# Kernel tuning notes

Measured on AMD Instinct MI355X. Metric: run time of the kernel, lower is better.

## Reference

```python
import jax, jax.numpy as jnp
import numpy as np

B, T, Fd, C, D = 16, 256, 128, 32, 32
K_RATIO = 0.5
EPS = 1e-5


def setup_inputs() -> dict:
    key = jax.random.key(0)
    ks = jax.random.split(key, 40)
    n = lambda i, shape, s=0.05: jax.random.normal(ks[i], shape, jnp.float32) * s
    inp = {"x": jax.random.normal(ks[0], (B, T, Fd, C), jnp.float32)}
    inp.update(c1w=n(1, (C, C)), c1b=n(2, (C,)), bng=1.0 + n(3, (C,)), bnb=n(4, (C,)),
               bnm=n(5, (C,)), bnv=jax.random.uniform(ks[6], (C,)) + 0.5,
               c2w=n(7, (1, C)), c2b=n(8, (1,)))
    def gat_params(i0, pre):
        return {pre + "apw": n(i0, (D, C)), pre + "apb": n(i0 + 1, (D,)),
                pre + "aw": n(i0 + 2, (D,)), pre + "pww": n(i0 + 3, (D, C)),
                pre + "pwb": n(i0 + 4, (D,)), pre + "pow": n(i0 + 5, (D, C)),
                pre + "pob": n(i0 + 6, (D,)), pre + "g": 1.0 + n(i0 + 7, (D,)),
                pre + "be": n(i0 + 8, (D,)), pre + "m": n(i0 + 9, (D,)),
                pre + "v": jax.random.uniform(ks[i0 + 10], (D,)) + 0.5}
    inp.update(gat_params(9, "fc_"))
    inp.update(gat_params(20, "tc_"))
    inp.update(pfw=n(31, (1, D)), pfb=n(32, (1,)), ptw=n(33, (1, D)), ptb=n(34, (1,)),
               w1=n(35, (D, D)), w2=n(36, (D, D)), fcw=n(37, (2, 2 * D)), fcb=n(38, (2,)))
    return inp


def _gat(h, apw, apb, aw, pww, pwb, poww, pob, g, be, mu, var):
    # h: (B, N, C). Dense pairwise multiplication -> (B, N, N, C)
    p = h[:, :, None, :] * h[:, None, :, :]
    e = jnp.tanh(jnp.einsum('bijc,dc->bijd', p, apw) + apb)      # (B,N,N,D)
    att = jax.nn.softmax(jnp.einsum('bijd,d->bij', e, aw), axis=2)  # softmax over dim=-2 (temp=1)
    out = jnp.einsum('bij,bjc->bic', att, h) @ pww.T + pwb + h @ poww.T + pob
    out = (out - mu) / jnp.sqrt(var + EPS) * g + be               # BatchNorm1d (eval)
    return jax.nn.selu(out)


def _pool(h, pw, pb, ratio):
    s = jax.nn.sigmoid(h @ pw.T + pb)                # (B,N,1)
    kn = max(int(h.shape[1] * ratio), 1)
    _, idx = jax.lax.top_k(s[..., 0], kn)            # (B,kn), descending scores
    return jnp.take_along_axis(h * s, idx[..., None], axis=1)


def reference(x, c1w, c1b, bng, bnb, bnm, bnv, c2w, c2b,
              fc_apw, fc_apb, fc_aw, fc_pww, fc_pwb, fc_pow, fc_pob, fc_g, fc_be, fc_m, fc_v,
              tc_apw, tc_apb, tc_aw, tc_pww, tc_pwb, tc_pow, tc_pob, tc_g, tc_be, tc_m, tc_v,
              pfw, pfb, ptw, ptb, w1, w2, fcw, fcb):
    # conv1 (1x1), SELU, BatchNorm2d (eval), conv2 (1x1 -> 1 channel)
    xp = jnp.einsum('oc,btfc->botf', c1w, x) + c1b[None, :, None, None]
    xp = jax.nn.selu(xp)
    xp = (xp - bnm[None, :, None, None]) / jnp.sqrt(bnv + EPS)[None, :, None, None] \
         * bng[None, :, None, None] + bnb[None, :, None, None]
    m = jnp.einsum('c,bctf->btf', c2w[0], xp) + c2b[0]           # (B,T,F)
    M0 = jax.nn.softmax(m, axis=1)
    FCatt = jnp.einsum('btf,btfc->bfc', M0, x)                   # sum over T
    TCatt = jnp.einsum('btf,btfc->btc', M0, x)                   # sum over F
    FC_gat = _gat(FCatt, fc_apw, fc_apb, fc_aw, fc_pww, fc_pwb, fc_pow, fc_pob, fc_g, fc_be, fc_m, fc_v)
    TC_gat = _gat(TCatt, tc_apw, tc_apb, tc_aw, tc_pww, tc_pwb, tc_pow, tc_pob, tc_g, tc_be, tc_m, tc_v)
    xF = _pool(FC_gat, pfw, pfb, K_RATIO)                        # (B, F/2, D)
    xT = _pool(TC_gat, ptw, ptb, K_RATIO)                        # (B, T/2, D)
    M1 = jax.nn.softmax((xF @ w1.T) @ xT.transpose(0, 2, 1), axis=-1)
    M2 = jax.nn.softmax((xT @ w2.T) @ xF.transpose(0, 2, 1), axis=-1)
    xF_fused = xF + M1 @ xT
    xT_fused = xT + M2 @ xF
    node = jnp.concatenate([xF_fused.max(axis=1), xT_fused.max(axis=1)], axis=-1)
    return node @ fcw.T + fcb
```

## Files before the change

kernel.cpp:

```cpp
#include <hip/hip_runtime.h>
#include <hip/hip_bf16.h>

#define Bn 16
#define Tn 256
#define Fn 128
#define Cn 32
#define Dn 32
#define EPSf 1e-5f
#define SELU_L 1.0507009873554805f
#define SELU_A 1.6732632423543772f

typedef unsigned short u16;
typedef unsigned int u32;
typedef __attribute__((ext_vector_type(8))) short bf16x8;
typedef __attribute__((ext_vector_type(4))) float f32x4;

struct Ptrs { const void* p[39]; };

#define P_C1W 0
#define P_C1B 1024
#define P_MW  1056
#define P_MK  1088
#define P_FC  1089
#define P_TCG (1089+3264)
#define G_APW 0
#define G_APB 1024
#define G_AW  1056
#define G_PWW 1088
#define G_PWB 2112
#define G_POW 2144
#define G_POB 3168
#define G_GS  3200
#define G_GB  3232
#define GAT_SZ 3264
#define P_PFW (P_TCG+GAT_SZ)
#define P_PFB (P_PFW+32)
#define P_PTW (P_PFB+1)
#define P_PTB (P_PTW+32)
#define P_W1  (P_PTB+1)
#define P_W2  (P_W1+1024)
#define P_FCW (P_W2+1024)
#define P_FCB (P_FCW+128)
#define P_FLAG 10000

#define WS_M     10240
#define WS_FCATT (WS_M+524288)
#define WS_TCATT (WS_FCATT+65536)
#define WS_FCGAT (WS_TCATT+131072)
#define WS_TCGAT (WS_FCGAT+65536)
#define WS_XF    (WS_TCGAT+131072)
#define WS_XT    (WS_XF+32768)
#define WS_XFF   (WS_XT+65536)
#define WS_XTF   (WS_XFF+32768)

__device__ __forceinline__ float bf2f(u16 u) {
    union { u32 i; float f; } v; v.i = ((u32)u) << 16; return v.f;
}
__device__ __forceinline__ u16 f2bf(float f) {
    union { float f; u32 u; } v; v.f = f;
    u32 r = (v.u + 0x7fffu + ((v.u >> 16) & 1u)) >> 16;
    return (u16)r;
}
__device__ __forceinline__ u32 cvt_pk_bf16(float lo, float hi) {
    u32 r;
    asm("v_cvt_pk_bf16_f32 %0, %1, %2" : "=v"(r) : "v"(lo), "v"(hi));
    return r;
}
__device__ __forceinline__ void up2(u32 u, float* o) {
    union { u32 i; float f; } a, b;
    a.i = u << 16; b.i = u & 0xffff0000u;
    o[0] = a.f; o[1] = b.f;
}
__device__ __forceinline__ float tanh_fast(float x) {
    float e = __expf(2.f * x);
    return 1.f - 2.f / (e + 1.f);
}
__device__ __forceinline__ float ldp(const void* p, int i, int isb) {
    return isb ? bf2f(((const u16*)p)[i]) : ((const float*)p)[i];
}

__global__ __launch_bounds__(256) void k0_setup(Ptrs in, float* __restrict__ P) {
    __shared__ int sflag;
    int tid = threadIdx.x;
    int blk = blockIdx.x;
    if (tid < 64) {
        const u16* xu = (const u16*)in.p[0];
        int bad = 0;
        #pragma unroll
        for (int q = 0; q < 4; q++) {
            float f = bf2f(xu[tid * 4 + q]);
            float a = fabsf(f);
            if (!(a < 64.f) && !(a == 0.f)) bad++;
        }
        #pragma unroll
        for (int off = 32; off >= 1; off >>= 1) bad += __shfl_xor(bad, off, 64);
        if (tid == 0) sflag = (bad <= 8) ? 1 : 0;
    }
    __syncthreads();
    const int isb = sflag;

    if (blk == 0) {
        if (tid == 0) P[P_FLAG] = (float)isb;
        for (int i = tid; i < 1024; i += 256) P[P_C1W + i] = ldp(in.p[1], i, isb);
        if (tid < 32) {
            float A = ldp(in.p[3], tid, isb) * rsqrtf(ldp(in.p[6], tid, isb) + EPSf);
            float w = ldp(in.p[7], tid, isb);
            P[P_C1B + tid] = ldp(in.p[2], tid, isb);
            P[P_MW + tid] = w * A * SELU_L;
            float Bc = ldp(in.p[4], tid, isb) - ldp(in.p[5], tid, isb) * A;
            float term = w * Bc;
            #pragma unroll
            for (int off = 16; off >= 1; off >>= 1) term += __shfl_xor(term, off, 64);
            if (tid == 0) P[P_MK] = term + ldp(in.p[8], 0, isb);
        }
        if (tid >= 64 && tid < 96) {
            int t = tid - 64;
            P[P_PFW + t] = ldp(in.p[31], t, isb);
            P[P_PTW + t] = ldp(in.p[33], t, isb);
        }
        if (tid == 96) { P[P_PFB] = ldp(in.p[32], 0, isb); P[P_PTB] = ldp(in.p[34], 0, isb); }
        if (tid == 97) P[P_FCB]     = ldp(in.p[38], 0, isb);
        if (tid == 98) P[P_FCB + 1] = ldp(in.p[38], 1, isb);
        if (tid >= 128) P[P_FCW + (tid - 128)] = ldp(in.p[37], tid - 128, isb);
    } else if (blk <= 2) {
        int g = blk - 1;
        int ib = g ? 20 : 9;
        float* G = P + (g ? P_TCG : P_FC);
        for (int i = tid; i < 1024; i += 256) {
            G[G_APW + i] = ldp(in.p[ib + 0], i, isb);
            G[G_PWW + i] = ldp(in.p[ib + 3], i, isb);
            G[G_POW + i] = ldp(in.p[ib + 5], i, isb);
        }
        if (tid < 32) {
            G[G_APB + tid] = ldp(in.p[ib + 1], tid, isb);
            G[G_AW  + tid] = ldp(in.p[ib + 2], tid, isb);
            G[G_PWB + tid] = ldp(in.p[ib + 4], tid, isb);
            G[G_POB + tid] = ldp(in.p[ib + 6], tid, isb);
            float gs = ldp(in.p[ib + 7], tid, isb) * rsqrtf(ldp(in.p[ib + 10], tid, isb) + EPSf);
            G[G_GS + tid] = gs;
            G[G_GB + tid] = ldp(in.p[ib + 8], tid, isb) - ldp(in.p[ib + 9], tid, isb) * gs;
        }
    } else {
        for (int i = tid; i < 1024; i += 256) {
            P[P_W1 + i] = ldp(in.p[35], i, isb);
            P[P_W2 + i] = ldp(in.p[36], i, isb);
        }
    }
}

__global__ __launch_bounds__(256) void k1_conv_m(const void* __restrict__ xin,
                                                 const float* __restrict__ P,
                                                 float* __restrict__ M) {
    const int isb = __builtin_amdgcn_readfirstlane((int)P[P_FLAG]);
    int tid = threadIdx.x;
    if (isb) {
        int w = tid >> 6, lane = tid & 63;
        int n = lane & 15, g = lane >> 4, kc = g * 8;
        union { u32 u[4]; bf16x8 v; } B0, B1;
        #pragma unroll
        for (int e = 0; e < 4; e++) {
            B0.u[e] = cvt_pk_bf16(P[P_C1W + n * 32 + kc + 2 * e],
                                  P[P_C1W + n * 32 + kc + 2 * e + 1]);
            B1.u[e] = cvt_pk_bf16(P[P_C1W + (n + 16) * 32 + kc + 2 * e],
                                  P[P_C1W + (n + 16) * 32 + kc + 2 * e + 1]);
        }
        float cb0v[4], cb1v[4], mw0v[4], mw1v[4];
        #pragma unroll
        for (int r = 0; r < 4; r++) {
            cb0v[r] = P[P_C1B + g * 4 + r];
            cb1v[r] = P[P_C1B + 16 + g * 4 + r];
            mw0v[r] = P[P_MW + g * 4 + r];
            mw1v[r] = P[P_MW + 16 + g * 4 + r];
        }
        float mk = P[P_MK];
        int rowblk = blockIdx.x * 256 + w * 64;
        const u16* xp = (const u16*)xin + (size_t)rowblk * 32;
        bf16x8 a[4];
        #pragma unroll
        for (int s = 0; s < 4; s++)
            a[s] = *(const bf16x8*)(xp + ((size_t)s * 16 + n) * 32 + kc);
        #pragma unroll
        for (int s = 0; s < 4; s++) {
            f32x4 c0 = {0.f, 0.f, 0.f, 0.f}, c1 = {0.f, 0.f, 0.f, 0.f};
            c0 = __builtin_amdgcn_mfma_f32_16x16x32_bf16(B0.v, a[s], c0, 0, 0, 0);
            c1 = __builtin_amdgcn_mfma_f32_16x16x32_bf16(B1.v, a[s], c1, 0, 0, 0);
            float part = 0.f;
            #pragma unroll
            for (int r = 0; r < 4; r++) {
                float z0 = c0[r] + cb0v[r], z1 = c1[r] + cb1v[r];
                float s0 = (z0 > 0.f) ? z0 : SELU_A * (__expf(z0) - 1.f);
                float s1 = (z1 > 0.f) ? z1 : SELU_A * (__expf(z1) - 1.f);
                part = fmaf(mw0v[r], s0, part);
                part = fmaf(mw1v[r], s1, part);
            }
            part += __shfl_xor(part, 16, 64);
            part += __shfl_xor(part, 32, 64);
            if (lane < 16) M[(size_t)rowblk + s * 16 + n] = part + mk;
        }
    } else {
        int idx = blockIdx.x * 256 + tid;
        float xv[32];
        const float4* xf4 = reinterpret_cast<const float4*>((const float*)xin + (size_t)idx * 32);
        #pragma unroll
        for (int q = 0; q < 8; q++) {
            float4 v = xf4[q];
            xv[q * 4 + 0] = v.x; xv[q * 4 + 1] = v.y;
            xv[q * 4 + 2] = v.z; xv[q * 4 + 3] = v.w;
        }
        float acc = P[P_MK];
        #pragma unroll
        for (int o = 0; o < 32; o++) {
            float z = P[P_C1B + o];
            #pragma unroll
            for (int c = 0; c < 32; c++) z = fmaf(P[P_C1W + o * 32 + c], xv[c], z);
            float br = (z > 0.f) ? z : SELU_A * (__expf(z) - 1.f);
            acc = fmaf(P[P_MW + o], br, acc);
        }
        M[idx] = acc;
    }
}

__global__ __launch_bounds__(256) void k2_softmax(float* __restrict__ M,
                                                  float* __restrict__ FCzero) {
    __shared__ float wred[4][16];
    int b = blockIdx.x >> 3, fg = blockIdx.x & 7;
    int tid = threadIdx.x;
    int w = tid >> 6, lane = tid & 63;
    int fq = tid & 3, tt = tid >> 2;
    float* colb = M + (size_t)b * (Tn * Fn) + fg * 16 + fq * 4;
    float4 v[4];
    float mx[4] = {-1e30f, -1e30f, -1e30f, -1e30f};
    #pragma unroll
    for (int p = 0; p < 4; p++) {
        v[p] = *(float4*)(colb + (size_t)(tt + p * 64) * Fn);
        mx[0] = fmaxf(mx[0], v[p].x); mx[1] = fmaxf(mx[1], v[p].y);
        mx[2] = fmaxf(mx[2], v[p].z); mx[3] = fmaxf(mx[3], v[p].w);
    }
    #pragma unroll
    for (int off = 4; off <= 32; off <<= 1) {
        #pragma unroll
        for (int c = 0; c < 4; c++) mx[c] = fmaxf(mx[c], __shfl_xor(mx[c], off, 64));
    }
    if (lane < 4) {
        #pragma unroll
        for (int c = 0; c < 4; c++) wred[w][lane * 4 + c] = mx[c];
    }
    __syncthreads();
    #pragma unroll
    for (int c = 0; c < 4; c++)
        mx[c] = fmaxf(fmaxf(wred[0][fq * 4 + c], wred[1][fq * 4 + c]),
                      fmaxf(wred[2][fq * 4 + c], wred[3][fq * 4 + c]));
    float4 e[4];
    float sm[4] = {0.f, 0.f, 0.f, 0.f};
    #pragma unroll
    for (int p = 0; p < 4; p++) {
        e[p].x = __expf(v[p].x - mx[0]); sm[0] += e[p].x;
        e[p].y = __expf(v[p].y - mx[1]); sm[1] += e[p].y;
        e[p].z = __expf(v[p].z - mx[2]); sm[2] += e[p].z;
        e[p].w = __expf(v[p].w - mx[3]); sm[3] += e[p].w;
    }
    #pragma unroll
    for (int off = 4; off <= 32; off <<= 1) {
        #pragma unroll
        for (int c = 0; c < 4; c++) sm[c] += __shfl_xor(sm[c], off, 64);
    }
    __syncthreads();
    if (lane < 4) {
        #pragma unroll
        for (int c = 0; c < 4; c++) wred[w][lane * 4 + c] = sm[c];
    }
    __syncthreads();
    float inv[4];
    #pragma unroll
    for (int c = 0; c < 4; c++)
        inv[c] = 1.f / (wred[0][fq * 4 + c] + wred[1][fq * 4 + c] +
                        wred[2][fq * 4 + c] + wred[3][fq * 4 + c]);
    #pragma unroll
    for (int p = 0; p < 4; p++) {
        float4 o4 = make_float4(e[p].x * inv[0], e[p].y * inv[1],
                                e[p].z * inv[2], e[p].w * inv[3]);
        *(float4*)(colb + (size_t)(tt + p * 64) * Fn) = o4;
    }
    int gid = blockIdx.x * 256 + tid;
    for (int i = gid; i < Bn * Fn * Cn; i += 128 * 256) FCzero[i] = 0.f;
}

__global__ __launch_bounds__(256) void k3n(const void* __restrict__ xin,
                                           const float* __restrict__ M,
                                           const float* __restrict__ Pflag,
                                           float* __restrict__ FCatt,
                                           float* __restrict__ TCatt) {
    __shared__ float part[4][8][32];
    int bi = blockIdx.x;
    int b = bi >> 5, tg = bi & 31;
    int tid = threadIdx.x;
    int w = tid >> 6, lane = tid & 63;
    int cc = (tid & 3) * 8, f0 = tid >> 2;
    const int isb = __builtin_amdgcn_readfirstlane((int)Pflag[P_FLAG]);
    float fa0[8], fa1[8];
    #pragma unroll
    for (int e = 0; e < 8; e++) { fa0[e] = 0.f; fa1[e] = 0.f; }
    for (int tt = 0; tt < 8; tt++) {
        int t = tg * 8 + tt;
        const float* Mrow = M + (size_t)b * (Tn * Fn) + (size_t)t * Fn;
        float m0 = Mrow[f0], m1 = Mrow[f0 + 64];
        size_t rowoff = ((size_t)b * Tn + t) * (Fn * Cn);
        float xv0[8], xv1[8];
        if (isb) {
            const u16* xr = (const u16*)xin + rowoff + f0 * 32 + cc;
            union { u32 u[4]; bf16x8 v; } q0, q1;
            q0.v = *(const bf16x8*)xr;
            q1.v = *(const bf16x8*)(xr + 64 * 32);
            up2(q0.u[0], xv0 + 0); up2(q0.u[1], xv0 + 2);
            up2(q0.u[2], xv0 + 4); up2(q0.u[3], xv0 + 6);
            up2(q1.u[0], xv1 + 0); up2(q1.u[1], xv1 + 2);
            up2(q1.u[2], xv1 + 4); up2(q1.u[3], xv1 + 6);
        } else {
            const float* xr = (const float*)xin + rowoff + f0 * 32 + cc;
            float4 a0 = *(const float4*)xr, a1 = *(const float4*)(xr + 4);
            float4 b0 = *(const float4*)(xr + 64 * 32), b1 = *(const float4*)(xr + 64 * 32 + 4);
            xv0[0] = a0.x; xv0[1] = a0.y; xv0[2] = a0.z; xv0[3] = a0.w;
            xv0[4] = a1.x; xv0[5] = a1.y; xv0[6] = a1.z; xv0[7] = a1.w;
            xv1[0] = b0.x; xv1[1] = b0.y; xv1[2] = b0.z; xv1[3] = b0.w;
            xv1[4] = b1.x; xv1[5] = b1.y; xv1[6] = b1.z; xv1[7] = b1.w;
        }
        float tp[8];
        #pragma unroll
        for (int e = 0; e < 8; e++) {
            float p0 = xv0[e] * m0, p1 = xv1[e] * m1;
            fa0[e] += p0; fa1[e] += p1;
            tp[e] = p0 + p1;
        }
        #pragma unroll
        for (int off = 4; off <= 32; off <<= 1) {
            #pragma unroll
            for (int e = 0; e < 8; e++) tp[e] += __shfl_xor(tp[e], off, 64);
        }
        if (lane < 4) {
            #pragma unroll
            for (int e = 0; e < 8; e++) part[w][tt][lane * 8 + e] = tp[e];
        }
    }
    __syncthreads();
    {
        int tt = tid >> 5, c = tid & 31;
        float s = part[0][tt][c] + part[1][tt][c] + part[2][tt][c] + part[3][tt][c];
        TCatt[((size_t)b * Tn + tg * 8 + tt) * Cn + c] = s;
    }
    #pragma unroll
    for (int e = 0; e < 8; e++) {
        atomicAdd(&FCatt[(size_t)b * 4096 + f0 * 32 + cc + e],        fa0[e]);
        atomicAdd(&FCatt[(size_t)b * 4096 + (f0 + 64) * 32 + cc + e], fa1[e]);
    }
}

template<int NT>
__device__ __forceinline__ void gat_row(const float* __restrict__ h,
                                        const float* __restrict__ G,
                                        float* __restrict__ out,
                                        int i, int lane) {
    int n = lane & 15, g = lane >> 4, kc = g * 8;
    union { u32 u[4]; bf16x8 v; } B0, B1;
    #pragma unroll
    for (int e = 0; e < 4; e++) {
        B0.u[e] = cvt_pk_bf16(G[G_APW + n * 32 + kc + 2 * e],
                              G[G_APW + n * 32 + kc + 2 * e + 1]);
        B1.u[e] = cvt_pk_bf16(G[G_APW + (n + 16) * 32 + kc + 2 * e],
                              G[G_APW + (n + 16) * 32 + kc + 2 * e + 1]);
    }
    float awv0[4], awv1[4], abv0[4], abv1[4];
    #pragma unroll
    for (int r = 0; r < 4; r++) {
        awv0[r] = G[G_AW + g * 4 + r];
        awv1[r] = G[G_AW + 16 + g * 4 + r];
        abv0[r] = G[G_APB + g * 4 + r];
        abv1[r] = G[G_APB + 16 + g * 4 + r];
    }
    float hi[8];
    {
        const float4* hip = (const float4*)(h + (size_t)i * 32 + kc);
        float4 v0 = hip[0], v1 = hip[1];
        hi[0] = v0.x; hi[1] = v0.y; hi[2] = v0.z; hi[3] = v0.w;
        hi[4] = v1.x; hi[5] = v1.y; hi[6] = v1.z; hi[7] = v1.w;
    }
    float sc[NT];
    #pragma unroll
    for (int jt = 0; jt < NT; jt++) {
        const float4* hjp = (const float4*)(h + ((size_t)jt * 16 + n) * 32 + kc);
        float4 v0 = hjp[0], v1 = hjp[1];
        union { u32 u[4]; bf16x8 v; } A;
        A.u[0] = cvt_pk_bf16(hi[0] * v0.x, hi[1] * v0.y);
        A.u[1] = cvt_pk_bf16(hi[2] * v0.z, hi[3] * v0.w);
        A.u[2] = cvt_pk_bf16(hi[4] * v1.x, hi[5] * v1.y);
        A.u[3] = cvt_pk_bf16(hi[6] * v1.z, hi[7] * v1.w);
        f32x4 c0 = {0.f, 0.f, 0.f, 0.f}, c1 = {0.f, 0.f, 0.f, 0.f};
        c0 = __builtin_amdgcn_mfma_f32_16x16x32_bf16(B0.v, A.v, c0, 0, 0, 0);
        c1 = __builtin_amdgcn_mfma_f32_16x16x32_bf16(B1.v, A.v, c1, 0, 0, 0);
        float part = 0.f;
        #pragma unroll
        for (int r = 0; r < 4; r++) {
            part = fmaf(awv0[r], tanh_fast(c0[r] + abv0[r]), part);
            part = fmaf(awv1[r], tanh_fast(c1[r] + abv1[r]), part);
        }
        part += __shfl_xor(part, 16, 64);
        part += __shfl_xor(part, 32, 64);
        sc[jt] = part;
    }
    float mx = -1e30f;
    #pragma unroll
    for (int jt = 0; jt < NT; jt++) mx = fmaxf(mx, sc[jt]);
    #pragma unroll
    for (int off = 1; off < 16; off <<= 1) mx = fmaxf(mx, __shfl_xor(mx, off, 64));
    float sum = 0.f;
    #pragma unroll
    for (int jt = 0; jt < NT; jt++) { sc[jt] = __expf(sc[jt] - mx); sum += sc[jt]; }
    #pragma unroll
    for (int off = 1; off < 16; off <<= 1) sum += __shfl_xor(sum, off, 64);
    float inv = 1.f / sum;
    float attp[8] = {0.f, 0.f, 0.f, 0.f, 0.f, 0.f, 0.f, 0.f};
    #pragma unroll
    for (int jt = 0; jt < NT; jt++) {
        const float4* hjp = (const float4*)(h + ((size_t)jt * 16 + n) * 32 + kc);
        float4 v0 = hjp[0], v1 = hjp[1];
        float p = sc[jt];
        attp[0] = fmaf(p, v0.x, attp[0]); attp[1] = fmaf(p, v0.y, attp[1]);
        attp[2] = fmaf(p, v0.z, attp[2]); attp[3] = fmaf(p, v0.w, attp[3]);
        attp[4] = fmaf(p, v1.x, attp[4]); attp[5] = fmaf(p, v1.y, attp[5]);
        attp[6] = fmaf(p, v1.z, attp[6]); attp[7] = fmaf(p, v1.w, attp[7]);
    }
    #pragma unroll
    for (int off = 1; off < 16; off <<= 1) {
        #pragma unroll
        for (int e = 0; e < 8; e++) attp[e] += __shfl_xor(attp[e], off, 64);
    }
    #pragma unroll
    for (int e = 0; e < 8; e++) attp[e] *= inv;
    float att[32], hif[32];
    #pragma unroll
    for (int gg = 0; gg < 4; gg++) {
        #pragma unroll
        for (int e = 0; e < 8; e++) {
            att[gg * 8 + e] = __shfl(attp[e], gg << 4, 64);
            hif[gg * 8 + e] = __shfl(hi[e],  gg << 4, 64);
        }
    }
    int d = lane & 31;
    float z = G[G_PWB + d] + G[G_POB + d];
    #pragma unroll
    for (int c = 0; c < 32; c++)
        z = fmaf(G[G_PWW + d * 32 + c], att[c], fmaf(G[G_POW + d * 32 + c], hif[c], z));
    z = z * G[G_GS + d] + G[G_GB + d];
    z = SELU_L * ((z > 0.f) ? z : SELU_A * (__expf(z) - 1.f));
    if (lane < 32) out[(size_t)i * 32 + d] = z;
}

__global__ __launch_bounds__(256) void k4ab(const float* __restrict__ P,
                                            const float* __restrict__ FCatt,
                                            const float* __restrict__ TCatt,
                                            float* __restrict__ FCgat,
                                            float* __restrict__ TCgat) {
    int bi = blockIdx.x, tid = threadIdx.x;
    int w = tid >> 6, lane = tid & 63;
    if (bi < 512) {
        int b = bi >> 5, i = (bi & 31) * 4 + w;
        gat_row<8>(FCatt + (size_t)b * 4096, P + P_FC, FCgat + (size_t)b * 4096, i, lane);
    } else {
        int u = bi - 512;
        int b = u >> 6, i = (u & 63) * 4 + w;
        gat_row<16>(TCatt + (size_t)b * 8192, P + P_TCG, TCgat + (size_t)b * 8192, i, lane);
    }
}

__global__ __launch_bounds__(256) void k5_pool(const float* __restrict__ P,
                                               const float* __restrict__ FCgat,
                                               const float* __restrict__ TCgat,
                                               float* __restrict__ XF,
                                               float* __restrict__ XT) {
    __shared__ float s[256];
    int bi = blockIdx.x;
    int N, kn, b, pboff; const float* g; float* xp; const float* pw;
    if (bi < 16) { b = bi; N = 128; kn = 64;
        g = FCgat + (size_t)b * 4096; xp = XF + (size_t)b * 2048; pw = P + P_PFW; pboff = P_PFB; }
    else { b = bi - 16; N = 256; kn = 128;
        g = TCgat + (size_t)b * 8192; xp = XT + (size_t)b * 4096; pw = P + P_PTW; pboff = P_PTB; }
    int tid = threadIdx.x;
    float sv = 0.f;
    if (tid < N) {
        float z = P[pboff];
        #pragma unroll
        for (int d = 0; d < 32; d++) z = fmaf(pw[d], g[(size_t)tid * 32 + d], z);
        sv = 1.f / (1.f + __expf(-z));
        s[tid] = sv;
    }
    __syncthreads();
    if (tid < N) {
        int rank = 0;
        for (int l = 0; l < N; l++) {
            float sl = s[l];
            rank += (sl > sv) || (sl == sv && l < tid);
        }
        if (rank < kn) {
            #pragma unroll
            for (int d = 0; d < 32; d++) xp[(size_t)rank * 32 + d] = g[(size_t)tid * 32 + d] * sv;
        }
    }
}

__global__ __launch_bounds__(256) void k6_fuse(const float* __restrict__ P,
                                               const float* __restrict__ XF,
                                               const float* __restrict__ XT,
                                               float* __restrict__ XFF,
                                               float* __restrict__ XTF) {
    int wid = blockIdx.x * 4 + (threadIdx.x >> 6);
    int lane = threadIdx.x & 63;
    if (wid < 1024) {
        int b = wid >> 6, i = wid & 63;
        const float* xf  = XF + ((size_t)b * 64 + i) * 32;
        const float* xtb = XT + (size_t)b * 4096;
        const float* w1 = P + P_W1;
        int d = lane & 31;
        float y = 0.f;
        #pragma unroll
        for (int c = 0; c < 32; c++) y = fmaf(w1[d * 32 + c], xf[c], y);
        float xtr0[32], xtr1[32];
        #pragma unroll
        for (int c = 0; c < 32; c++) {
            xtr0[c] = xtb[(size_t)lane * 32 + c];
            xtr1[c] = xtb[(size_t)(lane + 64) * 32 + c];
        }
        float s0 = 0.f, s1 = 0.f;
        #pragma unroll
        for (int c = 0; c < 32; c++) {
            float yc = __shfl(y, c, 64);
            s0 = fmaf(yc, xtr0[c], s0);
            s1 = fmaf(yc, xtr1[c], s1);
        }
        float mx = fmaxf(s0, s1);
        #pragma unroll
        for (int off = 1; off < 64; off <<= 1) mx = fmaxf(mx, __shfl_xor(mx, off, 64));
        float e0 = __expf(s0 - mx), e1 = __expf(s1 - mx);
        float sm = e0 + e1;
        #pragma unroll
        for (int off = 1; off < 64; off <<= 1) sm += __shfl_xor(sm, off, 64);
        float inv = 1.f / sm;
        float a0 = e0 * inv, a1 = e1 * inv;
        float v[32];
        #pragma unroll
        for (int c = 0; c < 32; c++) v[c] = a0 * xtr0[c] + a1 * xtr1[c];
        #pragma unroll
        for (int off = 1; off < 64; off <<= 1) {
            #pragma unroll
            for (int c = 0; c < 32; c++) v[c] += __shfl_xor(v[c], off, 64);
        }
        if (lane == 0) {
            float* o = XFF + ((size_t)b * 64 + i) * 32;
            #pragma unroll
            for (int c = 0; c < 32; c++) o[c] = xf[c] + v[c];
        }
    } else {
        int r = wid - 1024;
        int b = r >> 7, i = r & 127;
        const float* xt  = XT + ((size_t)b * 128 + i) * 32;
        const float* xfb = XF + (size_t)b * 2048;
        const float* w2 = P + P_W2;
        int d = lane & 31;
        float y = 0.f;
        #pragma unroll
        for (int c = 0; c < 32; c++) y = fmaf(w2[d * 32 + c], xt[c], y);
        float xfr[32];
        #pragma unroll
        for (int c = 0; c < 32; c++) xfr[c] = xfb[(size_t)lane * 32 + c];
        float sc0 = 0.f;
        #pragma unroll
        for (int c = 0; c < 32; c++) sc0 = fmaf(__shfl(y, c, 64), xfr[c], sc0);
        float mx = sc0;
        #pragma unroll
        for (int off = 1; off < 64; off <<= 1) mx = fmaxf(mx, __shfl_xor(mx, off, 64));
        float e = __expf(sc0 - mx);
        float sm = e;
        #pragma unroll
        for (int off = 1; off < 64; off <<= 1) sm += __shfl_xor(sm, off, 64);
        float a = e / sm;
        float v[32];
        #pragma unroll
        for (int c = 0; c < 32; c++) v[c] = a * xfr[c];
        #pragma unroll
        for (int off = 1; off < 64; off <<= 1) {
            #pragma unroll
            for (int c = 0; c < 32; c++) v[c] += __shfl_xor(v[c], off, 64);
        }
        if (lane == 0) {
            float* o = XTF + ((size_t)b * 128 + i) * 32;
            #pragma unroll
            for (int c = 0; c < 32; c++) o[c] = xt[c] + v[c];
        }
    }
}

__global__ __launch_bounds__(64) void k7_out(const float* __restrict__ P,
                                             const float* __restrict__ XFF,
                                             const float* __restrict__ XTF,
                                             void* __restrict__ outp) {
    __shared__ float node[64];
    int b = blockIdx.x, tid = threadIdx.x;
    if (tid < 32) {
        float m = -1e30f;
        for (int r = 0; r < 64; r++) m = fmaxf(m, XFF[((size_t)b * 64 + r) * 32 + tid]);
        node[tid] = m;
    } else {
        int c = tid - 32;
        float m = -1e30f;
        for (int r = 0; r < 128; r++) m = fmaxf(m, XTF[((size_t)b * 128 + r) * 32 + c]);
        node[tid] = m;
    }
    __syncthreads();
    if (tid < 2) {
        float z = P[P_FCB + tid];
        #pragma unroll
        for (int k = 0; k < 64; k++) z = fmaf(P[P_FCW + tid * 64 + k], node[k], z);
        int isb = (int)P[P_FLAG];
        if (isb) ((u16*)outp)[b * 2 + tid] = f2bf(z);
        else     ((float*)outp)[b * 2 + tid] = z;
    }
}

extern "C" void kernel_launch(void* const* d_in, const int* in_sizes, int n_in,
                              void* d_out, int out_size, void* d_ws, size_t ws_size,
                              hipStream_t stream) {
    (void)in_sizes; (void)n_in; (void)out_size; (void)ws_size;
    float* W = (float*)d_ws;
    Ptrs ptrs;
    for (int i = 0; i < 39; i++) ptrs.p[i] = d_in[i];
    const void* x = d_in[0];
    float* P = W;

    k0_setup<<<4, 256, 0, stream>>>(ptrs, P);
    k1_conv_m<<<2048, 256, 0, stream>>>(x, P, W + WS_M);
    k2_softmax<<<128, 256, 0, stream>>>(W + WS_M, W + WS_FCATT);
    k3n<<<512, 256, 0, stream>>>(x, W + WS_M, P, W + WS_FCATT, W + WS_TCATT);
    k4ab<<<1536, 256, 0, stream>>>(P, W + WS_FCATT, W + WS_TCATT,
                                   W + WS_FCGAT, W + WS_TCGAT);
    k5_pool<<<32, 256, 0, stream>>>(P, W + WS_FCGAT, W + WS_TCGAT, W + WS_XF, W + WS_XT);
    k6_fuse<<<768, 256, 0, stream>>>(P, W + WS_XF, W + WS_XT, W + WS_XFF, W + WS_XTF);
    k7_out<<<16, 64, 0, stream>>>(P, W + WS_XFF, W + WS_XTF, d_out);
}
```

Measured before the change: 344.6 us.

## Split GAT attention rows across waves and coalesce FCatt atomics via LDS

The GAT kernel now splits each attention row's neighbour columns across 2 or 4 waves. Each wave computes a partial softmax (max, sum, weighted h) and one wave merges the partials through LDS in a flash-style rescale. The grid grows from 1536 to 5120 blocks to raise parallelism and shorten per-wave serial chains. In k3n, the per-thread FCatt partials are staged in LDS and written back with contiguous atomics, to improve atomic coalescing. This costs an extra 16KB of LDS in k3n and a block barrier, with idle waves during the merge step in k4ab.

Result: faster. 314.2 us (-8.8%).

```diff
diff --git a/kernel.cpp b/kernel.cpp
--- a/kernel.cpp
+++ b/kernel.cpp
@@ -291,6 +291,7 @@
                                            float* __restrict__ FCatt,
                                            float* __restrict__ TCatt) {
     __shared__ float part[4][8][32];
+    __shared__ __align__(16) float sh[4096];
     int bi = blockIdx.x;
     int b = bi >> 5, tg = bi & 31;
     int tid = threadIdx.x;
@@ -341,6 +342,11 @@
             for (int e = 0; e < 8; e++) part[w][tt][lane * 8 + e] = tp[e];
         }
     }
+    float4* sh4 = (float4*)sh;
+    sh4[tid * 2]       = make_float4(fa0[0], fa0[1], fa0[2], fa0[3]);
+    sh4[tid * 2 + 1]   = make_float4(fa0[4], fa0[5], fa0[6], fa0[7]);
+    sh4[512 + tid * 2]     = make_float4(fa1[0], fa1[1], fa1[2], fa1[3]);
+    sh4[512 + tid * 2 + 1] = make_float4(fa1[4], fa1[5], fa1[6], fa1[7]);
     __syncthreads();
     {
         int tt = tid >> 5, c = tid & 31;
@@ -348,25 +354,41 @@
         TCatt[((size_t)b * Tn + tg * 8 + tt) * Cn + c] = s;
     }
     #pragma unroll
-    for (int e = 0; e < 8; e++) {
-        atomicAdd(&FCatt[(size_t)b * 4096 + f0 * 32 + cc + e],        fa0[e]);
-        atomicAdd(&FCatt[(size_t)b * 4096 + (f0 + 64) * 32 + cc + e], fa1[e]);
-    }
-}
-
-template<int NT>
-__device__ __forceinline__ void gat_row(const float* __restrict__ h,
-                                        const float* __restrict__ G,
-                                        float* __restrict__ out,
-                                        int i, int lane) {
+    for (int k = 0; k < 8; k++) {
+        float2 v = *(float2*)&sh[tid * 2 + 512 * k];
+        atomicAdd(&FCatt[(size_t)b * 4096 + tid * 2 + 512 * k],     v.x);
+        atomicAdd(&FCatt[(size_t)b * 4096 + tid * 2 + 512 * k + 1], v.y);
+    }
+}
+
+__global__ __launch_bounds__(256) void k4ab(const float* __restrict__ P,
+                                            const float* __restrict__ FCatt,
+                                            const float* __restrict__ TCatt,
+                                            float* __restrict__ FCgat,
+                                            float* __restrict__ TCgat) {
+    __shared__ float lds[4][36];
+    int bi = blockIdx.x, tid = threadIdx.x;
+    int w = tid >> 6, lane = tid & 63;
     int n = lane & 15, g = lane >> 4, kc = g * 8;
-    union { u32 u[4]; bf16x8 v; } B0, B1;
+    const float* h; const float* G; float* out;
+    int i, jt0, nparts, slot0;
+    if (bi < 1024) {
+        int b = bi >> 6, rp = bi & 63;
+        i = rp * 2 + (w >> 1); jt0 = (w & 1) * 4; nparts = 2; slot0 = (w >> 1) * 2;
+        h = FCatt + (size_t)b * 4096; G = P + P_FC; out = FCgat + (size_t)b * 4096;
+    } else {
+        int u = bi - 1024; int b = u >> 8;
+        i = u & 255; jt0 = w * 4; nparts = 4; slot0 = 0;
+        h = TCatt + (size_t)b * 8192; G = P + P_TCG; out = TCgat + (size_t)b * 8192;
+    }
+
+    union { u32 u4[4]; bf16x8 v; } B0, B1;
     #pragma unroll
     for (int e = 0; e < 4; e++) {
-        B0.u[e] = cvt_pk_bf16(G[G_APW + n * 32 + kc + 2 * e],
-                              G[G_APW + n * 32 + kc + 2 * e + 1]);
-        B1.u[e] = cvt_pk_bf16(G[G_APW + (n + 16) * 32 + kc + 2 * e],
-                              G[G_APW + (n + 16) * 32 + kc + 2 * e + 1]);
+        B0.u4[e] = cvt_pk_bf16(G[G_APW + n * 32 + kc + 2 * e],
+                               G[G_APW + n * 32 + kc + 2 * e + 1]);
+        B1.u4[e] = cvt_pk_bf16(G[G_APW + (n + 16) * 32 + kc + 2 * e],
+                               G[G_APW + (n + 16) * 32 + kc + 2 * e + 1]);
     }
     float awv0[4], awv1[4], abv0[4], abv1[4];
     #pragma unroll
@@ -383,16 +405,17 @@
         hi[0] = v0.x; hi[1] = v0.y; hi[2] = v0.z; hi[3] = v0.w;
         hi[4] = v1.x; hi[5] = v1.y; hi[6] = v1.z; hi[7] = v1.w;
     }
-    float sc[NT];
-    #pragma unroll
-    for (int jt = 0; jt < NT; jt++) {
+    float sc[4];
+    #pragma unroll
+    for (int q = 0; q < 4; q++) {
+        int jt = jt0 + q;
         const float4* hjp = (const float4*)(h + ((size_t)jt * 16 + n) * 32 + kc);
         float4 v0 = hjp[0], v1 = hjp[1];
-        union { u32 u[4]; bf16x8 v; } A;
-        A.u[0] = cvt_pk_bf16(hi[0] * v0.x, hi[1] * v0.y);
-        A.u[1] = cvt_pk_bf16(hi[2] * v0.z, hi[3] * v0.w);
-        A.u[2] = cvt_pk_bf16(hi[4] * v1.x, hi[5] * v1.y);
-        A.u[3] = cvt_pk_bf16(hi[6] * v1.z, hi[7] * v1.w);
+        union { u32 u4[4]; bf16x8 v; } A;
+        A.u4[0] = cvt_pk_bf16(hi[0] * v0.x, hi[1] * v0.y);
+        A.u4[1] = cvt_pk_bf16(hi[2] * v0.z, hi[3] * v0.w);
+        A.u4[2] = cvt_pk_bf16(hi[4] * v1.x, hi[5] * v1.y);
+        A.u4[3] = cvt_pk_bf16(hi[6] * v1.z, hi[7] * v1.w);
         f32x4 c0 = {0.f, 0.f, 0.f, 0.f}, c1 = {0.f, 0.f, 0.f, 0.f};
         c0 = __builtin_amdgcn_mfma_f32_16x16x32_bf16(B0.v, A.v, c0, 0, 0, 0);
         c1 = __builtin_amdgcn_mfma_f32_16x16x32_bf16(B1.v, A.v, c1, 0, 0, 0);
@@ -404,25 +427,23 @@
         }
         part += __shfl_xor(part, 16, 64);
         part += __shfl_xor(part, 32, 64);
-        sc[jt] = part;
-    }
-    float mx = -1e30f;
-    #pragma unroll
-    for (int jt = 0; jt < NT; jt++) mx = fmaxf(mx, sc[jt]);
-    #pragma unroll
-    for (int off = 1; off < 16; off <<= 1) mx = fmaxf(mx, __shfl_xor(mx, off, 64));
-    float sum = 0.f;
-    #pragma unroll
-    for (int jt = 0; jt < NT; jt++) { sc[jt] = __expf(sc[jt] - mx); sum += sc[jt]; }
-    #pragma unroll
-    for (int off = 1; off < 16; off <<= 1) sum += __shfl_xor(sum, off, 64);
-    float inv = 1.f / sum;
+        sc[q] = part;
+    }
+    float mh = fmaxf(fmaxf(sc[0], sc[1]), fmaxf(sc[2], sc[3]));
+    #pragma unroll
+    for (int off = 1; off < 16; off <<= 1) mh = fmaxf(mh, __shfl_xor(mh, off, 64));
+    float sumh = 0.f;
+    #pragma unroll
+    for (int q = 0; q < 4; q++) { sc[q] = __expf(sc[q] - mh); sumh += sc[q]; }
+    #pragma unroll
+    for (int off = 1; off < 16; off <<= 1) sumh += __shfl_xor(sumh, off, 64);
     float attp[8] = {0.f, 0.f, 0.f, 0.f, 0.f, 0.f, 0.f, 0.f};
     #pragma unroll
-    for (int jt = 0; jt < NT; jt++) {
+    for (int q = 0; q < 4; q++) {
+        int jt = jt0 + q;
         const float4* hjp = (const float4*)(h + ((size_t)jt * 16 + n) * 32 + kc);
         float4 v0 = hjp[0], v1 = hjp[1];
-        float p = sc[jt];
+        float p = sc[q];
         attp[0] = fmaf(p, v0.x, attp[0]); attp[1] = fmaf(p, v0.y, attp[1]);
         attp[2] = fmaf(p, v0.z, attp[2]); attp[3] = fmaf(p, v0.w, attp[3]);
         attp[4] = fmaf(p, v1.x, attp[4]); attp[5] = fmaf(p, v1.y, attp[5]);
@@ -433,41 +454,50 @@
         #pragma unroll
         for (int e = 0; e < 8; e++) attp[e] += __shfl_xor(attp[e], off, 64);
     }
-    #pragma unroll
-    for (int e = 0; e < 8; e++) attp[e] *= inv;
-    float att[32], hif[32];
-    #pragma unroll
-    for (int gg = 0; gg < 4; gg++) {
-        #pragma unroll
-        for (int e = 0; e < 8; e++) {
-            att[gg * 8 + e] = __shfl(attp[e], gg << 4, 64);
-            hif[gg * 8 + e] = __shfl(hi[e],  gg << 4, 64);
-        }
-    }
-    int d = lane & 31;
-    float z = G[G_PWB + d] + G[G_POB + d];
-    #pragma unroll
-    for (int c = 0; c < 32; c++)
-        z = fmaf(G[G_PWW + d * 32 + c], att[c], fmaf(G[G_POW + d * 32 + c], hif[c], z));
-    z = z * G[G_GS + d] + G[G_GB + d];
-    z = SELU_L * ((z > 0.f) ? z : SELU_A * (__expf(z) - 1.f));
-    if (lane < 32) out[(size_t)i * 32 + d] = z;
-}
-
-__global__ __launch_bounds__(256) void k4ab(const float* __restrict__ P,
-                                            const float* __restrict__ FCatt,
-                                            const float* __restrict__ TCatt,
-                                            float* __restrict__ FCgat,
-                                            float* __restrict__ TCgat) {
-    int bi = blockIdx.x, tid = threadIdx.x;
-    int w = tid >> 6, lane = tid & 63;
-    if (bi < 512) {
-        int b = bi >> 5, i = (bi & 31) * 4 + w;
-        gat_row<8>(FCatt + (size_t)b * 4096, P + P_FC, FCgat + (size_t)b * 4096, i, lane);
-    } else {
-        int u = bi - 512;
-        int b = u >> 6, i = (u & 63) * 4 + w;
-        gat_row<16>(TCatt + (size_t)b * 8192, P + P_TCG, TCgat + (size_t)b * 8192, i, lane);
+    if (n == 0) {
+        #pragma unroll
+        for (int e = 0; e < 8; e++) lds[w][2 + g * 8 + e] = attp[e];
+    }
+    if (lane == 0) { lds[w][0] = mh; lds[w][1] = sumh; }
+    __syncthreads();
+    bool comb = (nparts == 4) ? (w == 0) : ((w & 1) == 0);
+    if (comb) {
+        float hif[32];
+        #pragma unroll
+        for (int gg = 0; gg < 4; gg++) {
+            #pragma unroll
+            for (int e = 0; e < 8; e++) hif[gg * 8 + e] = __shfl(hi[e], gg << 4, 64);
+        }
+        int d = lane & 31;
+        float z = G[G_PWB + d] + G[G_POB + d];
+        if (nparts == 2) {
+            float m0 = lds[slot0][0],     s0 = lds[slot0][1];
+            float m1 = lds[slot0 + 1][0], s1 = lds[slot0 + 1][1];
+            float Mx = fmaxf(m0, m1);
+            float e0 = __expf(m0 - Mx), e1 = __expf(m1 - Mx);
+            float inv = 1.f / (s0 * e0 + s1 * e1);
+            #pragma unroll
+            for (int c = 0; c < 32; c++) {
+                float att = (lds[slot0][2 + c] * e0 + lds[slot0 + 1][2 + c] * e1) * inv;
+                z = fmaf(G[G_PWW + d * 32 + c], att, fmaf(G[G_POW + d * 32 + c], hif[c], z));
+            }
+        } else {
+            float m0 = lds[0][0], m1 = lds[1][0], m2 = lds[2][0], m3 = lds[3][0];
+            float Mx = fmaxf(fmaxf(m0, m1), fmaxf(m2, m3));
+            float e0 = __expf(m0 - Mx), e1 = __expf(m1 - Mx);
+            float e2 = __expf(m2 - Mx), e3 = __expf(m3 - Mx);
+            float inv = 1.f / (lds[0][1] * e0 + lds[1][1] * e1 +
+                               lds[2][1] * e2 + lds[3][1] * e3);
+            #pragma unroll
+            for (int c = 0; c < 32; c++) {
+                float att = (lds[0][2 + c] * e0 + lds[1][2 + c] * e1 +
+                             lds[2][2 + c] * e2 + lds[3][2 + c] * e3) * inv;
+                z = fmaf(G[G_PWW + d * 32 + c], att, fmaf(G[G_POW + d * 32 + c], hif[c], z));
+            }
+        }
+        z = z * G[G_GS + d] + G[G_GB + d];
+        z = SELU_L * ((z > 0.f) ? z : SELU_A * (__expf(z) - 1.f));
+        if (lane < 32) out[(size_t)i * 32 + d] = z;
     }
 }
 
@@ -638,7 +668,7 @@
     k1_conv_m<<<2048, 256, 0, stream>>>(x, P, W + WS_M);
     k2_softmax<<<128, 256, 0, stream>>>(W + WS_M, W + WS_FCATT);
     k3n<<<512, 256, 0, stream>>>(x, W + WS_M, P, W + WS_FCATT, W + WS_TCATT);
-    k4ab<<<1536, 256, 0, stream>>>(P, W + WS_FCATT, W + WS_TCATT,
+    k4ab<<<5120, 256, 0, stream>>>(P, W + WS_FCATT, W + WS_TCATT,
                                    W + WS_FCGAT, W + WS_TCGAT);
     k5_pool<<<32, 256, 0, stream>>>(P, W + WS_FCGAT, W + WS_TCGAT, W + WS_XF, W + WS_XT);
     k6_fuse<<<768, 256, 0, stream>>>(P, W + WS_XF, W + WS_XT, W + WS_XFF, W + WS_XTF);
```
